# Kernel optimization log

Hardware: AMD Instinct MI355X
Metric: run time of the kernel (lower is better)

## Reference

```python
import jax, jax.numpy as jnp
import numpy as np

NEG = -1e9

def conv1x1(x, w, b):
    # x: [B,C,H,W], w: [O,C], b: [O]
    return jnp.einsum('bchw,oc->bohw', x, w) + b[None, :, None, None]


def setup_inputs() -> dict:
    key = jax.random.key(0)
    ks = jax.random.split(key, 12)
    B, C, H, W = 4, 512, 96, 96
    Cr = min(8, C // 8)  # = 8
    s = lambda fan: 1.0 / np.sqrt(fan)
    inp = {
        'x':   jax.random.normal(ks[0], (B, C, H, W), dtype=jnp.float32),
        'w_h': jax.random.normal(ks[1], (Cr, C), dtype=jnp.float32) * s(C),
        'b_h': jax.random.normal(ks[2], (Cr,), dtype=jnp.float32) * s(C),
        'w_w': jax.random.normal(ks[3], (Cr, C), dtype=jnp.float32) * s(C),
        'b_w': jax.random.normal(ks[4], (Cr,), dtype=jnp.float32) * s(C),
        'w_c': jax.random.normal(ks[5], (C, C), dtype=jnp.float32) * s(C),
        'b_c': jax.random.normal(ks[6], (C,), dtype=jnp.float32) * s(C),
        'w_o': jax.random.normal(ks[7], (C, C), dtype=jnp.float32) * s(C),
        'b_o': jax.random.normal(ks[8], (C,), dtype=jnp.float32) * s(C),
        # alpha/beta/gamma are nn.Parameter(zeros(1)); use small nonzero values
        # so all branches contribute to output/gradients.
        'alpha': jax.random.normal(ks[9], (1,), dtype=jnp.float32) * 0.1,
        'beta':  jax.random.normal(ks[10], (1,), dtype=jnp.float32) * 0.1,
        'gamma': jax.random.normal(ks[11], (1,), dtype=jnp.float32) * 0.1,
    }
    return inp


def reference(x, w_h, b_h, w_w, b_w, w_c, b_c, w_o, b_o, alpha, beta, gamma):
    B, C, H, W = x.shape
    f_hei = conv1x1(x, w_h, b_h)              # [B,Cr,H,W]
    Cr = f_hei.shape[1]
    # Faithful replication of torch permute/contiguous/view sequence
    # (the .view(B*W,-1,H) after permute reinterprets the (H,Cr) layout as (Cr,H)).
    f_h = f_hei.transpose(0, 3, 2, 1).reshape(B * W, Cr, H).transpose(0, 2, 1)  # [B*W,H,Cr]
    f_w = f_hei.transpose(0, 2, 1, 3).reshape(B * H, Cr, W).transpose(0, 2, 1)  # [B*H,W,Cr]
    f_wid = conv1x1(x, w_w, b_w)              # [B,Cr,H,W]
    ff_h = f_wid.transpose(0, 3, 1, 2).reshape(B * W, Cr, H)  # [B*W,Cr,H]
    ff_w = f_wid.transpose(0, 2, 1, 3).reshape(B * H, Cr, W)  # [B*H,Cr,W]
    # channel attention branch
    f_ch = conv1x1(x, w_c, b_c)               # [B,C,H,W]
    f_c = f_ch.reshape(B, C, H * W)           # [B,C,HW]
    ff_c = f_ch.transpose(0, 2, 3, 1).reshape(B, H * W, C)    # [B,HW,C]
    aff_c = jax.nn.softmax(jnp.matmul(f_c, ff_c), axis=2)     # [B,C,C]
    out_C = jnp.matmul(ff_c, aff_c).reshape(B, C, H, W)       # torch .view reinterpretation
    # axial (criss-cross) attention with masked concat-softmax
    E_h = jnp.matmul(f_h, ff_h)               # [B*W,H,H]
    E_h = E_h + (jnp.eye(H, dtype=x.dtype) * NEG)[None, :, :]
    E_h = E_h.reshape(B, W, H, H).transpose(0, 2, 1, 3)       # [B,H,W,H]
    E_w = jnp.matmul(f_w, ff_w).reshape(B, H, W, W)           # [B,H,W,W]
    concate = jax.nn.softmax(jnp.concatenate([E_h, E_w], axis=3), axis=3)  # [B,H,W,H+W]
    h_att = concate[:, :, :, :H].transpose(0, 2, 1, 3).reshape(B * W, H, H)
    w_att = concate[:, :, :, H:].reshape(B * H, W, W)
    f_cha = conv1x1(x, w_o, b_o)              # [B,C,H,W]
    P_H = f_cha.transpose(0, 3, 1, 2).reshape(B * W, C, H)
    P_W = f_cha.transpose(0, 2, 1, 3).reshape(B * H, C, W)
    out_H = jnp.matmul(P_H, h_att.transpose(0, 2, 1)).reshape(B, W, C, H).transpose(0, 2, 3, 1)
    out_W = jnp.matmul(P_W, w_att.transpose(0, 2, 1)).reshape(B, H, C, W).transpose(0, 2, 1, 3)
    return x + alpha * out_H + beta * out_W + gamma * out_C
```

## Files before the change

### kernel.cpp

```cpp
#include <hip/hip_runtime.h>

typedef __attribute__((ext_vector_type(8))) short short8;
typedef __attribute__((ext_vector_type(4))) float f32x4;
typedef __attribute__((ext_vector_type(4))) unsigned short us4;
typedef unsigned short u16;

#define kB 4
#define kC 512
#define kCr 8
#define kH 96
#define kW 96
#define kHW 9216
#define kCHW 4718592
#define NEGV -1e9f

__device__ __forceinline__ u16 f2b(float f) {
  union { float f; unsigned u; } v; v.f = f;
  unsigned r = v.u + 0x7fff + ((v.u >> 16) & 1);
  return (u16)(r >> 16);
}
__device__ __forceinline__ float b2f(u16 h) {
  union { unsigned u; float f; } v; v.u = ((unsigned)h) << 16;
  return v.f;
}
#define MFMA(a, b, c) __builtin_amdgcn_mfma_f32_16x16x32_bf16(a, b, c, 0, 0, 0)

__device__ __forceinline__ void gl16(const u16* g, u16* l) {
  __builtin_amdgcn_global_load_lds(
      (const __attribute__((address_space(1))) void*)g,
      (__attribute__((address_space(3))) void*)l, 16, 0, 0);
}

__global__ __launch_bounds__(256) void k_cvt_T(const float* __restrict__ in,
                                               u16* __restrict__ out,
                                               int R, int C) {
  const float* ib = in + (size_t)blockIdx.z * R * C;
  u16* ob = out + (size_t)blockIdx.z * R * C;
  int c0 = blockIdx.x * 64, r0 = blockIdx.y * 64;
  __shared__ u16 T[64][68];
  int tid = threadIdx.x;
#pragma unroll
  for (int p = 0; p < 4; p++) {
    int ch = tid + p * 256;
    int i = ch >> 4, seg = ch & 15;
    f32x4 v = *(const f32x4*)&ib[(size_t)(r0 + i) * C + c0 + seg * 4];
    T[i][seg*4+0] = f2b(v[0]); T[i][seg*4+1] = f2b(v[1]);
    T[i][seg*4+2] = f2b(v[2]); T[i][seg*4+3] = f2b(v[3]);
  }
  __syncthreads();
#pragma unroll
  for (int p = 0; p < 4; p++) {
    int ch = tid + p * 256;
    int j = ch >> 4, seg = ch & 15;
    us4 o;
#pragma unroll
    for (int e = 0; e < 4; e++) o[e] = T[seg*4+e][j];
    *(us4*)&ob[(size_t)(c0 + j) * R + r0 + seg * 4] = o;
  }
}

__global__ __launch_bounds__(256) void k_trT_bf(const u16* __restrict__ in,
                                                u16* __restrict__ out,
                                                int R, int C) {
  const u16* ib = in + (size_t)blockIdx.z * R * C;
  u16* ob = out + (size_t)blockIdx.z * R * C;
  int c0 = blockIdx.x * 64, r0 = blockIdx.y * 64;
  __shared__ u16 T[64][68];
  int tid = threadIdx.x;
#pragma unroll
  for (int p = 0; p < 4; p++) {
    int ch = tid + p * 256;
    int i = ch >> 4, seg = ch & 15;
    us4 v = *(const us4*)&ib[(size_t)(r0 + i) * C + c0 + seg * 4];
    T[i][seg*4+0] = v[0]; T[i][seg*4+1] = v[1];
    T[i][seg*4+2] = v[2]; T[i][seg*4+3] = v[3];
  }
  __syncthreads();
#pragma unroll
  for (int p = 0; p < 4; p++) {
    int ch = tid + p * 256;
    int j = ch >> 4, seg = ch & 15;
    us4 o;
#pragma unroll
    for (int e = 0; e < 4; e++) o[e] = T[seg*4+e][j];
    *(us4*)&ob[(size_t)(c0 + j) * R + r0 + seg * 4] = o;
  }
}

__global__ __launch_bounds__(256) void k_cvtw(const float* __restrict__ wc,
                                              const float* __restrict__ wo,
                                              u16* __restrict__ wco) {
  int i = blockIdx.x * 256 + threadIdx.x;
  const float* src = (i < 65536) ? &wc[(size_t)i * 4] : &wo[(size_t)(i - 65536) * 4];
  f32x4 v = *(const f32x4*)src;
  us4 o;
  o[0] = f2b(v[0]); o[1] = f2b(v[1]); o[2] = f2b(v[2]); o[3] = f2b(v[3]);
  ((us4*)wco)[i] = o;
}

__global__ __launch_bounds__(256) void k_conv16(
    const float* __restrict__ wh, const float* __restrict__ bh,
    const float* __restrict__ ww, const float* __restrict__ bw,
    const u16* __restrict__ XT, u16* __restrict__ Out) {
  __shared__ u16 As[16][520];
  __shared__ float bias_s[16];
  int tid = threadIdx.x;
#pragma unroll
  for (int p = 0; p < 4; p++) {
    int ch = tid + p * 256;
    int r = ch >> 6, seg = ch & 63;
    const float* src = (r < 8) ? &wh[r * 512 + seg * 8] : &ww[(r - 8) * 512 + seg * 8];
    f32x4 v0 = *(const f32x4*)src;
    f32x4 v1 = *(const f32x4*)(src + 4);
    short8 sv;
    sv[0]=f2b(v0[0]); sv[1]=f2b(v0[1]); sv[2]=f2b(v0[2]); sv[3]=f2b(v0[3]);
    sv[4]=f2b(v1[0]); sv[5]=f2b(v1[1]); sv[6]=f2b(v1[2]); sv[7]=f2b(v1[3]);
    *(short8*)&As[r][seg * 8] = sv;
  }
  if (tid < 16) bias_s[tid] = (tid < 8) ? bh[tid] : bw[tid - 8];
  __syncthreads();
  int b = blockIdx.y;
  int nb = blockIdx.x * 128 + (tid >> 6) * 32;
  int lane = tid & 63;
  int lr = lane & 15, lg = lane >> 4;
  const u16* Bb = XT + (size_t)b * kCHW;
  f32x4 acc[2] = {};
#pragma unroll 4
  for (int k0 = 0; k0 < 512; k0 += 32) {
    short8 a = *(const short8*)&As[lr][k0 + lg * 8];
    short8 b0 = *(const short8*)&Bb[(size_t)(nb + lr) * 512 + k0 + lg * 8];
    short8 b1 = *(const short8*)&Bb[(size_t)(nb + 16 + lr) * 512 + k0 + lg * 8];
    acc[0] = MFMA(a, b0, acc[0]);
    acc[1] = MFMA(a, b1, acc[1]);
  }
#pragma unroll
  for (int q = 0; q < 2; q++)
#pragma unroll
    for (int r = 0; r < 4; r++) {
      int m = lg * 4 + r;
      Out[((size_t)b * 16 + m) * kHW + nb + q * 16 + lr] = f2b(acc[q][r] + bias_s[m]);
    }
}

#define GEMM_PROLOG()                                                      \
  int tid = threadIdx.x;                                                   \
  int lane = tid & 63, wv = tid >> 6;                                      \
  int wr = (wv >> 1) * 64, wc = (wv & 1) * 64;                             \
  int lr = lane & 15, lg = lane >> 4;                                      \
  f32x4 acc[4][4] = {};

#define STAGE(bufv, kk)                                                    \
  {                                                                        \
    _Pragma("unroll")                                                      \
    for (int p = 0; p < 4; p++) {                                          \
      int ch = tid + p * 256;                                              \
      int row = ch >> 3, cc = ch & 7;                                      \
      int sc = (cc ^ (row & 7)) * 8;                                       \
      gl16(&Asrc[(size_t)(bm + row) * LDA + (kk) + sc], &As[bufv][row][cc * 8]); \
      gl16(&Bsrc[(size_t)(bn + row) * LDB + (kk) + sc], &Bs[bufv][row][cc * 8]); \
    }                                                                      \
  }

#define COMPUTE(bufv)                                                      \
  {                                                                        \
    _Pragma("unroll")                                                      \
    for (int ks = 0; ks < 2; ks++) {                                       \
      int ca = ((ks * 4 + lg) ^ (lr & 7)) * 8;                             \
      short8 av[4], bv[4];                                                 \
      _Pragma("unroll")                                                    \
      for (int m = 0; m < 4; m++)                                          \
        av[m] = *(const short8*)&As[bufv][wr + m * 16 + lr][ca];           \
      _Pragma("unroll")                                                    \
      for (int n = 0; n < 4; n++)                                          \
        bv[n] = *(const short8*)&Bs[bufv][wc + n * 16 + lr][ca];           \
      __builtin_amdgcn_s_setprio(1);                                       \
      _Pragma("unroll")                                                    \
      for (int m = 0; m < 4; m++)                                          \
        _Pragma("unroll")                                                  \
        for (int n = 0; n < 4; n++)                                        \
          acc[m][n] = MFMA(av[m], bv[n], acc[m][n]);                       \
      __builtin_amdgcn_s_setprio(0);                                       \
    }                                                                      \
  }

#define VMBAR(N)                                                           \
  asm volatile("s_waitcnt vmcnt(" #N ")" ::: "memory");                    \
  __builtin_amdgcn_s_barrier();

#define LGBAR                                                              \
  asm volatile("s_waitcnt lgkmcnt(0)" ::: "memory");                       \
  __builtin_amdgcn_s_barrier();

#define PIPELOOP(NT, KBASE)                                                \
  STAGE(0, (KBASE));                                                       \
  STAGE(1, (KBASE) + 64);                                                  \
  {                                                                        \
    int cur = 0;                                                           \
    _Pragma("unroll 1")                                                    \
    for (int t = 0; t < (NT) - 2; t++) {                                   \
      VMBAR(8);                                                            \
      COMPUTE(cur);                                                        \
      LGBAR;                                                               \
      STAGE(cur, (KBASE) + (t + 2) * 64);                                  \
      cur ^= 1;                                                            \
    }                                                                      \
    VMBAR(8);                                                              \
    COMPUTE(cur);                                                          \
    cur ^= 1;                                                              \
    VMBAR(0);                                                              \
    COMPUTE(cur);                                                          \
  }

__global__ __launch_bounds__(256) void k_gemm_conv2(
    const u16* __restrict__ wco, const u16* __restrict__ BT,
    const float* __restrict__ b_c, const float* __restrict__ b_o,
    u16* __restrict__ f_ch, u16* __restrict__ f_cha) {
  __shared__ u16 As[2][128][64];
  __shared__ u16 Bs[2][128][64];
  int b = blockIdx.z;
  int bm = blockIdx.y * 128;
  int bn = blockIdx.x * 128;
  const u16* Asrc = wco;
  const u16* Bsrc = BT + (size_t)b * kCHW;
  const int LDA = 512, LDB = 512;
  GEMM_PROLOG();
  PIPELOOP(8, 0);
  const float* biasp = (bm < 512) ? (b_c + bm) : (b_o + bm - 512);
  u16* Ob = (bm < 512) ? (f_ch + (size_t)b * kCHW + (size_t)bm * kHW)
                       : (f_cha + (size_t)b * kCHW + (size_t)(bm - 512) * kHW);
#pragma unroll
  for (int m = 0; m < 4; m++)
#pragma unroll
    for (int r = 0; r < 4; r++) {
      int ol = wr + m * 16 + lg * 4 + r;
      float bv_ = biasp[ol];
#pragma unroll
      for (int n = 0; n < 4; n++)
        Ob[(size_t)ol * kHW + bn + wc + n * 16 + lr] = f2b(acc[m][n][r] + bv_);
    }
}

__global__ __launch_bounds__(256) void k_gram_sk(const u16* __restrict__ F,
                                                 u16* __restrict__ part) {
  __shared__ u16 As[2][128][64];
  __shared__ u16 Bs[2][128][64];
  int z = blockIdx.z;
  int b = z & 3, s = z >> 2;
  int bm = blockIdx.y * 128, bn = blockIdx.x * 128;
  const u16* Asrc = F + (size_t)b * kCHW;
  const u16* Bsrc = Asrc;
  const int LDA = kHW, LDB = kHW;
  int kbeg = s * 1152;
  GEMM_PROLOG();
  PIPELOOP(18, kbeg);
  u16* Pb = part + ((size_t)(s * 4 + b)) * 262144;
#pragma unroll
  for (int m = 0; m < 4; m++)
#pragma unroll
    for (int r = 0; r < 4; r++) {
      int i = bm + wr + m * 16 + lg * 4 + r;
#pragma unroll
      for (int n = 0; n < 4; n++)
        Pb[(size_t)i * 512 + bn + wc + n * 16 + lr] = f2b(acc[m][n][r]);
    }
}

__global__ __launch_bounds__(256) void k_outc(
    const u16* __restrict__ AT, const u16* __restrict__ Bt,
    const float* __restrict__ gamma, u16* __restrict__ Out) {
  __shared__ u16 As[2][128][64];
  __shared__ u16 Bs[2][128][64];
  int b = blockIdx.z;
  int bm = blockIdx.y * 128;
  int bn = blockIdx.x * 128;
  const u16* Asrc = AT + (size_t)b * kCHW;
  const u16* Bsrc = Bt + (size_t)b * 262144;
  const int LDA = 512, LDB = 512;
  GEMM_PROLOG();
  PIPELOOP(8, 0);
  float g = *gamma;
  u16* Ob = Out + (size_t)b * kCHW;
#pragma unroll
  for (int m = 0; m < 4; m++)
#pragma unroll
    for (int r = 0; r < 4; r++) {
      int mm = bm + wr + m * 16 + lg * 4 + r;
#pragma unroll
      for (int n = 0; n < 4; n++)
        Ob[(size_t)mm * 512 + bn + wc + n * 16 + lr] = f2b(g * acc[m][n][r]);
    }
}

__global__ __launch_bounds__(256) void k_softmax512r(const u16* __restrict__ part,
                                                     float* __restrict__ gramN) {
  int b = blockIdx.x >> 9, i = blockIdx.x & 511;
  int tid = threadIdx.x;
  float v0 = 0.f, v1 = 0.f;
#pragma unroll
  for (int s = 0; s < 8; s++) {
    const u16* P = part + ((size_t)(s * 4 + b) * 512 + i) * 512;
    v0 += b2f(P[tid]);
    v1 += b2f(P[tid + 256]);
  }
  int wid = tid >> 6, lane = tid & 63;
  float m = fmaxf(v0, v1);
#pragma unroll
  for (int o = 32; o >= 1; o >>= 1) m = fmaxf(m, __shfl_xor(m, o));
  __shared__ float redm[4], reds[4];
  if (lane == 0) redm[wid] = m;
  __syncthreads();
  m = fmaxf(fmaxf(redm[0], redm[1]), fmaxf(redm[2], redm[3]));
  float e0 = expf(v0 - m), e1 = expf(v1 - m);
  float s = e0 + e1;
#pragma unroll
  for (int o = 32; o >= 1; o >>= 1) s += __shfl_xor(s, o);
  if (lane == 0) reds[wid] = s;
  __syncthreads();
  s = reds[0] + reds[1] + reds[2] + reds[3];
  float inv = 1.0f / s;
  float* R = gramN + ((size_t)b * 512 + i) * 512;
  R[tid] = e0 * inv;
  R[tid + 256] = e1 * inv;
}

__global__ __launch_bounds__(256) void k_eh(
    const u16* __restrict__ fhw, u16* __restrict__ Ccat) {
  int b = blockIdx.x / kW, w = blockIdx.x % kW;
  __shared__ float fh[kH][kCr];
  __shared__ float fw[kCr][kH];
  int tid = threadIdx.x;
  for (int l = tid; l < kH * kCr; l += 256) {
    int i = l >> 3, c = l & 7;
    fh[i][c] = b2f(fhw[((size_t)b * 16 + (i & 7)) * kHW + (c * 12 + (i >> 3)) * kW + w]);
    int c2 = l / kH, j = l % kH;
    fw[c2][j] = b2f(fhw[((size_t)b * 16 + 8 + c2) * kHW + j * kW + w]);
  }
  __syncthreads();
  for (int t = tid; t < kH * kH; t += 256) {
    int i = t / kH, j = t % kH;
    float e = 0.f;
#pragma unroll
    for (int c = 0; c < kCr; c++) e += fh[i][c] * fw[c][j];
    if (i == j) e += NEGV;
    Ccat[(((size_t)b * kH + i) * kW + w) * 192 + j] = f2b(e);
  }
}

__global__ __launch_bounds__(256) void k_ew(
    const u16* __restrict__ fhw, u16* __restrict__ Ccat) {
  int b = blockIdx.x / kH, h = blockIdx.x % kH;
  __shared__ float fh2[kCr][kW];
  __shared__ float fw2[kCr][kW];
  int tid = threadIdx.x;
  for (int l = tid; l < kCr * kW; l += 256) {
    int c = l / kW, w = l % kW;
    fh2[c][w] = b2f(fhw[((size_t)b * 16 + c) * kHW + h * kW + w]);
    fw2[c][w] = b2f(fhw[((size_t)b * 16 + 8 + c) * kHW + h * kW + w]);
  }
  __syncthreads();
  for (int t = tid; t < kW * kW; t += 256) {
    int w = t / kW, j = t % kW;
    float e = 0.f;
#pragma unroll
    for (int c = 0; c < kCr; c++) e += fh2[c][w] * fw2[c][j];
    Ccat[(((size_t)b * kH + h) * kW + w) * 192 + 96 + j] = f2b(e);
  }
}

__global__ __launch_bounds__(256) void k_softmax192(u16* __restrict__ Ccat) {
  int r = blockIdx.x * 4 + (threadIdx.x >> 6);
  int lane = threadIdx.x & 63;
  u16* R = Ccat + (size_t)r * 192;
  float a = b2f(R[lane]), b = b2f(R[lane + 64]), c = b2f(R[lane + 128]);
  float m = fmaxf(a, fmaxf(b, c));
#pragma unroll
  for (int o = 32; o >= 1; o >>= 1) m = fmaxf(m, __shfl_xor(m, o));
  float ea = expf(a - m), eb = expf(b - m), ec = expf(c - m);
  float s = ea + eb + ec;
#pragma unroll
  for (int o = 32; o >= 1; o >>= 1) s += __shfl_xor(s, o);
  float inv = 1.0f / s;
  R[lane] = f2b(ea * inv);
  R[lane + 64] = f2b(eb * inv);
  R[lane + 128] = f2b(ec * inv);
}

__global__ __launch_bounds__(256) void k_tr_plane(const u16* __restrict__ in,
                                                  u16* __restrict__ out) {
  size_t pl = blockIdx.x;
  const u16* ib = in + pl * 9216;
  u16* ob = out + pl * 9216;
  __shared__ u16 T[96][100];
  int tid = threadIdx.x;
  for (int ch = tid; ch < 96 * 24; ch += 256) {
    int i = ch / 24, seg = ch % 24;
    *(us4*)&T[i][seg*4] = *(const us4*)&ib[i*96 + seg*4];
  }
  __syncthreads();
  for (int ch = tid; ch < 96 * 24; ch += 256) {
    int j = ch / 24, seg = ch % 24;
    us4 o;
#pragma unroll
    for (int e = 0; e < 4; e++) o[e] = T[seg*4+e][j];
    *(us4*)&ob[j*96 + seg*4] = o;
  }
}

__global__ __launch_bounds__(512) void k_final_h(
    const u16* __restrict__ AT,
    const u16* __restrict__ att,
    const float* __restrict__ alpha,
    u16* __restrict__ OutHT) {
  int b = blockIdx.x / 96, w = blockIdx.x % 96;
  __shared__ u16 Bs[96][104];
  int tid = threadIdx.x;
  for (int ch = tid; ch < 1152; ch += 512) {
    int h = ch / 12, seg = ch % 12;
    *(short8*)&Bs[h][seg*8] =
        *(const short8*)&att[(((size_t)b*96 + h)*96 + w)*192 + seg*8];
  }
  __syncthreads();
  int lane = tid & 63, wv = tid >> 6;
  int lr = lane & 15, lg = lane >> 4;
  int c0 = wv * 64;
  const u16* Ab = AT + ((size_t)b*512 + c0)*kHW + w*96;
  f32x4 acc[4][6] = {};
#pragma unroll
  for (int ks = 0; ks < 3; ks++) {
    short8 av[4];
#pragma unroll
    for (int m = 0; m < 4; m++)
      av[m] = *(const short8*)&Ab[(size_t)(m*16 + lr)*kHW + ks*32 + lg*8];
#pragma unroll
    for (int n = 0; n < 6; n++) {
      short8 bv = *(const short8*)&Bs[n*16 + lr][ks*32 + lg*8];
#pragma unroll
      for (int m = 0; m < 4; m++) acc[m][n] = MFMA(av[m], bv, acc[m][n]);
    }
  }
  float al = *alpha;
  u16* Ob = OutHT + ((size_t)b*512 + c0)*kHW + w*96;
#pragma unroll
  for (int m = 0; m < 4; m++)
#pragma unroll
    for (int r = 0; r < 4; r++) {
      size_t crow = (size_t)(m*16 + lg*4 + r) * kHW;
#pragma unroll
      for (int n = 0; n < 6; n++)
        Ob[crow + n*16 + lr] = f2b(al * acc[m][n][r]);
    }
}

__global__ __launch_bounds__(512) void k_final_w(
    const u16* __restrict__ A,
    const u16* __restrict__ att,
    const float* __restrict__ beta,
    u16* __restrict__ OutW) {
  int b = blockIdx.x / 96, h = blockIdx.x % 96;
  __shared__ u16 Bs[96][104];
  int tid = threadIdx.x;
  for (int ch = tid; ch < 1152; ch += 512) {
    int wr_ = ch / 12, seg = ch % 12;
    *(short8*)&Bs[wr_][seg*8] =
        *(const short8*)&att[(((size_t)b*96 + h)*96 + wr_)*192 + 96 + seg*8];
  }
  __syncthreads();
  int lane = tid & 63, wv = tid >> 6;
  int lr = lane & 15, lg = lane >> 4;
  int c0 = wv * 64;
  const u16* Ab = A + ((size_t)b*512 + c0)*kHW + h*96;
  f32x4 acc[4][6] = {};
#pragma unroll
  for (int ks = 0; ks < 3; ks++) {
    short8 av[4];
#pragma unroll
    for (int m = 0; m < 4; m++)
      av[m] = *(const short8*)&Ab[(size_t)(m*16 + lr)*kHW + ks*32 + lg*8];
#pragma unroll
    for (int n = 0; n < 6; n++) {
      short8 bv = *(const short8*)&Bs[n*16 + lr][ks*32 + lg*8];
#pragma unroll
      for (int m = 0; m < 4; m++) acc[m][n] = MFMA(av[m], bv, acc[m][n]);
    }
  }
  float be = *beta;
  u16* Ob = OutW + ((size_t)b*512 + c0)*kHW + h*96;
#pragma unroll
  for (int m = 0; m < 4; m++)
#pragma unroll
    for (int r = 0; r < 4; r++) {
      size_t crow = (size_t)(m*16 + lg*4 + r) * kHW;
#pragma unroll
      for (int n = 0; n < 6; n++)
        Ob[crow + n*16 + lr] = f2b(be * acc[m][n][r]);
    }
}

__global__ __launch_bounds__(256) void k_merge(
    const float* __restrict__ x, const u16* __restrict__ OutC,
    const u16* __restrict__ OutW, const u16* __restrict__ HT,
    float* __restrict__ out) {
  size_t pl = blockIdx.x;
  const u16* hb = HT + pl * 9216;
  __shared__ u16 T[96][100];
  int tid = threadIdx.x;
  for (int ch = tid; ch < 96 * 24; ch += 256) {
    int i = ch / 24, seg = ch % 24;
    *(us4*)&T[i][seg*4] = *(const us4*)&hb[i*96 + seg*4];
  }
  __syncthreads();
  const float* xb = x + pl * 9216;
  const u16* cb = OutC + pl * 9216;
  const u16* wb = OutW + pl * 9216;
  float* ob = out + pl * 9216;
  for (int ch = tid; ch < 2304; ch += 256) {
    int i4 = ch * 4;
    int h = i4 / 96, w = i4 % 96;
    f32x4 xv = *(const f32x4*)&xb[i4];
    us4 cv = *(const us4*)&cb[i4];
    us4 wv = *(const us4*)&wb[i4];
    f32x4 o;
#pragma unroll
    for (int e = 0; e < 4; e++)
      o[e] = xv[e] + b2f(cv[e]) + b2f(wv[e]) + b2f(T[w + e][h]);
    *(f32x4*)&ob[i4] = o;
  }
}

extern "C" void kernel_launch(void* const* d_in, const int* in_sizes, int n_in,
                              void* d_out, int out_size, void* d_ws, size_t ws_size,
                              hipStream_t stream) {
  const float* x     = (const float*)d_in[0];
  const float* w_h   = (const float*)d_in[1];
  const float* b_h   = (const float*)d_in[2];
  const float* w_w   = (const float*)d_in[3];
  const float* b_w   = (const float*)d_in[4];
  const float* w_c   = (const float*)d_in[5];
  const float* b_c   = (const float*)d_in[6];
  const float* w_o   = (const float*)d_in[7];
  const float* b_o   = (const float*)d_in[8];
  const float* alpha = (const float*)d_in[9];
  const float* beta  = (const float*)d_in[10];
  const float* gamma = (const float*)d_in[11];
  float* out = (float*)d_out;

  const size_t R = 37748736;
  char* p = (char*)d_ws;
  u16*   xbfT   = (u16*)(p);
  u16*   part   = (u16*)(p);
  u16*   f_chaT = (u16*)(p);
  u16*   outW   = (u16*)(p);
  u16*   f_ch   = (u16*)(p + R);
  u16*   outC   = (u16*)(p + R);
  u16*   f_chT  = (u16*)(p + 2 * R);
  u16*   outHT  = (u16*)(p + 2 * R);
  u16*   f_cha  = (u16*)(p + 3 * R);
  u16*   fhw    = (u16*)(p + 4 * R);
  char*  F      = p + 4 * R + 2359296;
  float* gramN  = (float*)F;
  u16*   affT   = (u16*)(F + 4194304);
  u16*   ccat   = (u16*)F;
  u16*   wco    = (u16*)(F + 14155776);

  k_cvt_T<<<dim3(144, 8, 4), 256, 0, stream>>>(x, xbfT, 512, 9216);
  k_cvtw<<<512, 256, 0, stream>>>(w_c, w_o, wco);
  k_conv16<<<dim3(72, 4), 256, 0, stream>>>(w_h, b_h, w_w, b_w, xbfT, fhw);
  k_gemm_conv2<<<dim3(72, 8, 4), 256, 0, stream>>>(wco, xbfT, b_c, b_o, f_ch, f_cha);
  k_trT_bf<<<dim3(144, 8, 4), 256, 0, stream>>>(f_ch, f_chT, 512, 9216);
  k_gram_sk<<<dim3(4, 4, 32), 256, 0, stream>>>(f_ch, part);
  k_softmax512r<<<2048, 256, 0, stream>>>(part, gramN);
  k_cvt_T<<<dim3(8, 8, 4), 256, 0, stream>>>(gramN, affT, 512, 512);
  k_outc<<<dim3(4, 72, 4), 256, 0, stream>>>(f_chT, affT, gamma, outC);
  k_eh<<<384, 256, 0, stream>>>(fhw, ccat);
  k_ew<<<384, 256, 0, stream>>>(fhw, ccat);
  k_softmax192<<<9216, 256, 0, stream>>>(ccat);
  k_tr_plane<<<2048, 256, 0, stream>>>(f_cha, f_chaT);
  k_final_h<<<384, 512, 0, stream>>>(f_chaT, ccat, alpha, outHT);
  k_final_w<<<384, 512, 0, stream>>>(f_cha, ccat, beta, outW);
  k_merge<<<2048, 256, 0, stream>>>(x, outC, outW, outHT, out);
}
```

Before: 304.9 us.

## Fuse f_ch transpose into conv GEMM, exploit Gram symmetry, widen N tiles

The channel conv GEMM now loops over four 128-wide N segments per block and writes both f_ch and its transpose directly from registers. This removes the separate k_trT_bf transpose pass over a 4.7M-element tensor per batch. The Gram split-K kernel computes only the upper-triangular 128x128 tiles (10 of 16) and mirrors the off-diagonal ones with transposed stores. k_outc processes two N segments per block so the pipeline prologue is amortized. The costs are strided transposed stores that may coalesce poorly and fewer blocks per launch.

```diff
diff --git a/kernel.cpp b/kernel.cpp
--- a/kernel.cpp
+++ b/kernel.cpp
@@ -46,34 +46,6 @@
     f32x4 v = *(const f32x4*)&ib[(size_t)(r0 + i) * C + c0 + seg * 4];
     T[i][seg*4+0] = f2b(v[0]); T[i][seg*4+1] = f2b(v[1]);
     T[i][seg*4+2] = f2b(v[2]); T[i][seg*4+3] = f2b(v[3]);
-  }
-  __syncthreads();
-#pragma unroll
-  for (int p = 0; p < 4; p++) {
-    int ch = tid + p * 256;
-    int j = ch >> 4, seg = ch & 15;
-    us4 o;
-#pragma unroll
-    for (int e = 0; e < 4; e++) o[e] = T[seg*4+e][j];
-    *(us4*)&ob[(size_t)(c0 + j) * R + r0 + seg * 4] = o;
-  }
-}
-
-__global__ __launch_bounds__(256) void k_trT_bf(const u16* __restrict__ in,
-                                                u16* __restrict__ out,
-                                                int R, int C) {
-  const u16* ib = in + (size_t)blockIdx.z * R * C;
-  u16* ob = out + (size_t)blockIdx.z * R * C;
-  int c0 = blockIdx.x * 64, r0 = blockIdx.y * 64;
-  __shared__ u16 T[64][68];
-  int tid = threadIdx.x;
-#pragma unroll
-  for (int p = 0; p < 4; p++) {
-    int ch = tid + p * 256;
-    int i = ch >> 4, seg = ch & 15;
-    us4 v = *(const us4*)&ib[(size_t)(r0 + i) * C + c0 + seg * 4];
-    T[i][seg*4+0] = v[0]; T[i][seg*4+1] = v[1];
-    T[i][seg*4+2] = v[2]; T[i][seg*4+3] = v[3];
   }
   __syncthreads();
 #pragma unroll
@@ -214,30 +186,69 @@
 __global__ __launch_bounds__(256) void k_gemm_conv2(
     const u16* __restrict__ wco, const u16* __restrict__ BT,
     const float* __restrict__ b_c, const float* __restrict__ b_o,
-    u16* __restrict__ f_ch, u16* __restrict__ f_cha) {
+    u16* __restrict__ f_ch, u16* __restrict__ f_cha, u16* __restrict__ f_chT) {
   __shared__ u16 As[2][128][64];
   __shared__ u16 Bs[2][128][64];
   int b = blockIdx.z;
   int bm = blockIdx.y * 128;
-  int bn = blockIdx.x * 128;
+  int bn0 = blockIdx.x * 512;
   const u16* Asrc = wco;
   const u16* Bsrc = BT + (size_t)b * kCHW;
-  const int LDA = 512, LDB = 512;
   GEMM_PROLOG();
-  PIPELOOP(8, 0);
   const float* biasp = (bm < 512) ? (b_c + bm) : (b_o + bm - 512);
+  float bias_r[16];
+#pragma unroll
+  for (int m = 0; m < 4; m++)
+#pragma unroll
+    for (int r = 0; r < 4; r++)
+      bias_r[m * 4 + r] = biasp[wr + m * 16 + lg * 4 + r];
   u16* Ob = (bm < 512) ? (f_ch + (size_t)b * kCHW + (size_t)bm * kHW)
                        : (f_cha + (size_t)b * kCHW + (size_t)(bm - 512) * kHW);
-#pragma unroll
-  for (int m = 0; m < 4; m++)
-#pragma unroll
-    for (int r = 0; r < 4; r++) {
-      int ol = wr + m * 16 + lg * 4 + r;
-      float bv_ = biasp[ol];
-#pragma unroll
-      for (int n = 0; n < 4; n++)
-        Ob[(size_t)ol * kHW + bn + wc + n * 16 + lr] = f2b(acc[m][n][r] + bv_);
-    }
+  u16* Tb = f_chT + (size_t)b * kCHW;
+
+#define C2_STAGE(bufv, t)                                                  \
+  {                                                                        \
+    int seg_ = (t) >> 3, kk_ = ((t) & 7) * 64;                             \
+    int bn_ = bn0 + seg_ * 128;                                            \
+    _Pragma("unroll")                                                      \
+    for (int p = 0; p < 4; p++) {                                          \
+      int ch = tid + p * 256;                                              \
+      int row = ch >> 3, cc = ch & 7;                                      \
+      int sc = (cc ^ (row & 7)) * 8;                                       \
+      gl16(&Asrc[(size_t)(bm + row) * 512 + kk_ + sc], &As[bufv][row][cc * 8]); \
+      gl16(&Bsrc[(size_t)(bn_ + row) * 512 + kk_ + sc], &Bs[bufv][row][cc * 8]); \
+    }                                                                      \
+  }
+
+  C2_STAGE(0, 0);
+  C2_STAGE(1, 1);
+  int cur = 0;
+#pragma unroll 1
+  for (int t = 0; t < 32; t++) {
+    if (t < 31) { VMBAR(8); } else { VMBAR(0); }
+    COMPUTE(cur);
+    if (t < 30) { LGBAR; C2_STAGE(cur, t + 2); }
+    cur ^= 1;
+    if ((t & 7) == 7) {
+      int bn = bn0 + (t >> 3) * 128;
+#pragma unroll
+      for (int m = 0; m < 4; m++)
+#pragma unroll
+        for (int n = 0; n < 4; n++) {
+          us4 tv;
+#pragma unroll
+          for (int r = 0; r < 4; r++) {
+            float v = acc[m][n][r] + bias_r[m * 4 + r];
+            tv[r] = f2b(v);
+            Ob[(size_t)(wr + m * 16 + lg * 4 + r) * kHW + bn + wc + n * 16 + lr] = tv[r];
+            acc[m][n][r] = 0.f;
+          }
+          if (bm < 512)
+            *(us4*)&Tb[(size_t)(bn + wc + n * 16 + lr) * 512 + bm + wr + m * 16 + lg * 4] = tv;
+        }
+    }
+  }
+#undef C2_STAGE
 }
 
 __global__ __launch_bounds__(256) void k_gram_sk(const u16* __restrict__ F,
@@ -246,7 +257,9 @@
   __shared__ u16 Bs[2][128][64];
   int z = blockIdx.z;
   int b = z & 3, s = z >> 2;
-  int bm = blockIdx.y * 128, bn = blockIdx.x * 128;
+  int L = blockIdx.x;
+  int bm = (int)((0x3221110000ull >> (4 * L)) & 15) * 128;
+  int bn = (int)((0x3323213210ull >> (4 * L)) & 15) * 128;
   const u16* Asrc = F + (size_t)b * kCHW;
   const u16* Bsrc = Asrc;
   const int LDA = kHW, LDB = kHW;
@@ -257,11 +270,15 @@
 #pragma unroll
   for (int m = 0; m < 4; m++)
 #pragma unroll
-    for (int r = 0; r < 4; r++) {
-      int i = bm + wr + m * 16 + lg * 4 + r;
-#pragma unroll
-      for (int n = 0; n < 4; n++)
-        Pb[(size_t)i * 512 + bn + wc + n * 16 + lr] = f2b(acc[m][n][r]);
+    for (int n = 0; n < 4; n++) {
+      us4 tv;
+#pragma unroll
+      for (int r = 0; r < 4; r++) {
+        tv[r] = f2b(acc[m][n][r]);
+        Pb[(size_t)(bm + wr + m * 16 + lg * 4 + r) * 512 + bn + wc + n * 16 + lr] = tv[r];
+      }
+      if (bm != bn)
+        *(us4*)&Pb[(size_t)(bn + wc + n * 16 + lr) * 512 + bm + wr + m * 16 + lg * 4] = tv;
     }
 }
 
@@ -272,23 +289,52 @@
   __shared__ u16 Bs[2][128][64];
   int b = blockIdx.z;
   int bm = blockIdx.y * 128;
-  int bn = blockIdx.x * 128;
+  int bn0 = blockIdx.x * 256;
   const u16* Asrc = AT + (size_t)b * kCHW;
   const u16* Bsrc = Bt + (size_t)b * 262144;
-  const int LDA = 512, LDB = 512;
   GEMM_PROLOG();
-  PIPELOOP(8, 0);
   float g = *gamma;
   u16* Ob = Out + (size_t)b * kCHW;
-#pragma unroll
-  for (int m = 0; m < 4; m++)
-#pragma unroll
-    for (int r = 0; r < 4; r++) {
-      int mm = bm + wr + m * 16 + lg * 4 + r;
-#pragma unroll
-      for (int n = 0; n < 4; n++)
-        Ob[(size_t)mm * 512 + bn + wc + n * 16 + lr] = f2b(g * acc[m][n][r]);
-    }
+
+#define OC_STAGE(bufv, t)                                                  \
+  {                                                                        \
+    int seg_ = (t) >> 3, kk_ = ((t) & 7) * 64;                             \
+    int bn_ = bn0 + seg_ * 128;                                            \
+    _Pragma("unroll")                                                      \
+    for (int p = 0; p < 4; p++) {                                          \
+      int ch = tid + p * 256;                                              \
+      int row = ch >> 3, cc = ch & 7;                                      \
+      int sc = (cc ^ (row & 7)) * 8;                                       \
+      gl16(&Asrc[(size_t)(bm + row) * 512 + kk_ + sc], &As[bufv][row][cc * 8]); \
+      gl16(&Bsrc[(size_t)(bn_ + row) * 512 + kk_ + sc], &Bs[bufv][row][cc * 8]); \
+    }                                                                      \
+  }
+
+  OC_STAGE(0, 0);
+  OC_STAGE(1, 1);
+  int cur = 0;
+#pragma unroll 1
+  for (int t = 0; t < 16; t++) {
+    if (t < 15) { VMBAR(8); } else { VMBAR(0); }
+    COMPUTE(cur);
+    if (t < 14) { LGBAR; OC_STAGE(cur, t + 2); }
+    cur ^= 1;
+    if ((t & 7) == 7) {
+      int bn = bn0 + (t >> 3) * 128;
+#pragma unroll
+      for (int m = 0; m < 4; m++)
+#pragma unroll
+        for (int r = 0; r < 4; r++) {
+          int mm = bm + wr + m * 16 + lg * 4 + r;
+#pragma unroll
+          for (int n = 0; n < 4; n++) {
+            Ob[(size_t)mm * 512 + bn + wc + n * 16 + lr] = f2b(g * acc[m][n][r]);
+            acc[m][n][r] = 0.f;
+          }
+        }
+    }
+  }
+#undef OC_STAGE
 }
 
 __global__ __launch_bounds__(256) void k_softmax512r(const u16* __restrict__ part,
@@ -565,12 +611,11 @@
   k_cvt_T<<<dim3(144, 8, 4), 256, 0, stream>>>(x, xbfT, 512, 9216);
   k_cvtw<<<512, 256, 0, stream>>>(w_c, w_o, wco);
   k_conv16<<<dim3(72, 4), 256, 0, stream>>>(w_h, b_h, w_w, b_w, xbfT, fhw);
-  k_gemm_conv2<<<dim3(72, 8, 4), 256, 0, stream>>>(wco, xbfT, b_c, b_o, f_ch, f_cha);
-  k_trT_bf<<<dim3(144, 8, 4), 256, 0, stream>>>(f_ch, f_chT, 512, 9216);
-  k_gram_sk<<<dim3(4, 4, 32), 256, 0, stream>>>(f_ch, part);
+  k_gemm_conv2<<<dim3(18, 8, 4), 256, 0, stream>>>(wco, xbfT, b_c, b_o, f_ch, f_cha, f_chT);
+  k_gram_sk<<<dim3(10, 1, 32), 256, 0, stream>>>(f_ch, part);
   k_softmax512r<<<2048, 256, 0, stream>>>(part, gramN);
   k_cvt_T<<<dim3(8, 8, 4), 256, 0, stream>>>(gramN, affT, 512, 512);
-  k_outc<<<dim3(4, 72, 4), 256, 0, stream>>>(f_chT, affT, gamma, outC);
+  k_outc<<<dim3(2, 72, 4), 256, 0, stream>>>(f_chT, affT, gamma, outC);
   k_eh<<<384, 256, 0, stream>>>(fhw, ccat);
   k_ew<<<384, 256, 0, stream>>>(fhw, ccat);
   k_softmax192<<<9216, 256, 0, stream>>>(ccat);
```

Result: slower. 337.0 us (+10.5%).

## Fuse f_ch transpose into conv GEMM epilogue and exploit Gram symmetry

Applied to the files above, without the earlier changes.

The conv GEMM epilogue now also writes a transposed copy of f_ch through shared memory, which removes the separate k_trT_bf transpose kernel and its extra read/write pass. The Gram split-K kernel computes only the upper-triangular 128x128 tiles (10 of 16) and mirrors each tile into its symmetric position, cutting its MFMA work. The costs are a larger epilogue with extra syncs and LDS traffic in the conv kernel, and uncoalesced mirrored stores in the Gram kernel. The tvals array is computed but never used.

```diff
diff --git a/kernel.cpp b/kernel.cpp
--- a/kernel.cpp
+++ b/kernel.cpp
@@ -46,34 +46,6 @@
     f32x4 v = *(const f32x4*)&ib[(size_t)(r0 + i) * C + c0 + seg * 4];
     T[i][seg*4+0] = f2b(v[0]); T[i][seg*4+1] = f2b(v[1]);
     T[i][seg*4+2] = f2b(v[2]); T[i][seg*4+3] = f2b(v[3]);
-  }
-  __syncthreads();
-#pragma unroll
-  for (int p = 0; p < 4; p++) {
-    int ch = tid + p * 256;
-    int j = ch >> 4, seg = ch & 15;
-    us4 o;
-#pragma unroll
-    for (int e = 0; e < 4; e++) o[e] = T[seg*4+e][j];
-    *(us4*)&ob[(size_t)(c0 + j) * R + r0 + seg * 4] = o;
-  }
-}
-
-__global__ __launch_bounds__(256) void k_trT_bf(const u16* __restrict__ in,
-                                                u16* __restrict__ out,
-                                                int R, int C) {
-  const u16* ib = in + (size_t)blockIdx.z * R * C;
-  u16* ob = out + (size_t)blockIdx.z * R * C;
-  int c0 = blockIdx.x * 64, r0 = blockIdx.y * 64;
-  __shared__ u16 T[64][68];
-  int tid = threadIdx.x;
-#pragma unroll
-  for (int p = 0; p < 4; p++) {
-    int ch = tid + p * 256;
-    int i = ch >> 4, seg = ch & 15;
-    us4 v = *(const us4*)&ib[(size_t)(r0 + i) * C + c0 + seg * 4];
-    T[i][seg*4+0] = v[0]; T[i][seg*4+1] = v[1];
-    T[i][seg*4+2] = v[2]; T[i][seg*4+3] = v[3];
   }
   __syncthreads();
 #pragma unroll
@@ -214,9 +186,10 @@
 __global__ __launch_bounds__(256) void k_gemm_conv2(
     const u16* __restrict__ wco, const u16* __restrict__ BT,
     const float* __restrict__ b_c, const float* __restrict__ b_o,
-    u16* __restrict__ f_ch, u16* __restrict__ f_cha) {
-  __shared__ u16 As[2][128][64];
-  __shared__ u16 Bs[2][128][64];
+    u16* __restrict__ f_ch, u16* __restrict__ f_cha, u16* __restrict__ f_chT) {
+  __shared__ u16 smem[32768];
+  u16 (*As)[128][64] = (u16 (*)[128][64])smem;
+  u16 (*Bs)[128][64] = (u16 (*)[128][64])(smem + 16384);
   int b = blockIdx.z;
   int bm = blockIdx.y * 128;
   int bn = blockIdx.x * 128;
@@ -228,6 +201,7 @@
   const float* biasp = (bm < 512) ? (b_c + bm) : (b_o + bm - 512);
   u16* Ob = (bm < 512) ? (f_ch + (size_t)b * kCHW + (size_t)bm * kHW)
                        : (f_cha + (size_t)b * kCHW + (size_t)(bm - 512) * kHW);
+  u16 tvals[4][4];
 #pragma unroll
   for (int m = 0; m < 4; m++)
 #pragma unroll
@@ -235,9 +209,37 @@
       int ol = wr + m * 16 + lg * 4 + r;
       float bv_ = biasp[ol];
 #pragma unroll
-      for (int n = 0; n < 4; n++)
-        Ob[(size_t)ol * kHW + bn + wc + n * 16 + lr] = f2b(acc[m][n][r] + bv_);
-    }
+      for (int n = 0; n < 4; n++) {
+        u16 hv = f2b(acc[m][n][r] + bv_);
+        Ob[(size_t)ol * kHW + bn + wc + n * 16 + lr] = hv;
+        tvals[m][n] = (r == 0) ? hv : tvals[m][n];
+      }
+    }
+  if (bm < 512) {
+    __syncthreads();
+    u16 (*T)[136] = (u16 (*)[136])smem;
+#pragma unroll
+    for (int m = 0; m < 4; m++)
+#pragma unroll
+      for (int n = 0; n < 4; n++) {
+        int ol = wr + m * 16 + lg * 4;
+        float bv0 = biasp[ol], bv1 = biasp[ol+1], bv2 = biasp[ol+2], bv3 = biasp[ol+3];
+        int nl = wc + n * 16 + lr;
+        T[nl][ol + 0] = f2b(acc[m][n][0] + bv0);
+        T[nl][ol + 1] = f2b(acc[m][n][1] + bv1);
+        T[nl][ol + 2] = f2b(acc[m][n][2] + bv2);
+        T[nl][ol + 3] = f2b(acc[m][n][3] + bv3);
+      }
+    __syncthreads();
+    u16* Tb = f_chT + (size_t)b * kCHW;
+#pragma unroll
+    for (int p = 0; p < 16; p++) {
+      int ch = tid + p * 256;
+      int row = ch >> 5, seg = ch & 31;
+      us4 v = *(const us4*)&T[row][seg * 4];
+      *(us4*)&Tb[(size_t)(bn + row) * 512 + bm + seg * 4] = v;
+    }
+  }
 }
 
 __global__ __launch_bounds__(256) void k_gram_sk(const u16* __restrict__ F,
@@ -246,7 +248,9 @@
   __shared__ u16 Bs[2][128][64];
   int z = blockIdx.z;
   int b = z & 3, s = z >> 2;
-  int bm = blockIdx.y * 128, bn = blockIdx.x * 128;
+  int L = blockIdx.x;
+  int bm = (int)((0x3221110000ull >> (4 * L)) & 15) * 128;
+  int bn = (int)((0x3323213210ull >> (4 * L)) & 15) * 128;
   const u16* Asrc = F + (size_t)b * kCHW;
   const u16* Bsrc = Asrc;
   const int LDA = kHW, LDB = kHW;
@@ -257,11 +261,15 @@
 #pragma unroll
   for (int m = 0; m < 4; m++)
 #pragma unroll
-    for (int r = 0; r < 4; r++) {
-      int i = bm + wr + m * 16 + lg * 4 + r;
-#pragma unroll
-      for (int n = 0; n < 4; n++)
-        Pb[(size_t)i * 512 + bn + wc + n * 16 + lr] = f2b(acc[m][n][r]);
+    for (int n = 0; n < 4; n++) {
+      us4 tv;
+#pragma unroll
+      for (int r = 0; r < 4; r++) {
+        tv[r] = f2b(acc[m][n][r]);
+        Pb[(size_t)(bm + wr + m * 16 + lg * 4 + r) * 512 + bn + wc + n * 16 + lr] = tv[r];
+      }
+      if (bm != bn)
+        *(us4*)&Pb[(size_t)(bn + wc + n * 16 + lr) * 512 + bm + wr + m * 16 + lg * 4] = tv;
     }
 }
 
@@ -565,9 +573,8 @@
   k_cvt_T<<<dim3(144, 8, 4), 256, 0, stream>>>(x, xbfT, 512, 9216);
   k_cvtw<<<512, 256, 0, stream>>>(w_c, w_o, wco);
   k_conv16<<<dim3(72, 4), 256, 0, stream>>>(w_h, b_h, w_w, b_w, xbfT, fhw);
-  k_gemm_conv2<<<dim3(72, 8, 4), 256, 0, stream>>>(wco, xbfT, b_c, b_o, f_ch, f_cha);
-  k_trT_bf<<<dim3(144, 8, 4), 256, 0, stream>>>(f_ch, f_chT, 512, 9216);
-  k_gram_sk<<<dim3(4, 4, 32), 256, 0, stream>>>(f_ch, part);
+  k_gemm_conv2<<<dim3(72, 8, 4), 256, 0, stream>>>(wco, xbfT, b_c, b_o, f_ch, f_cha, f_chT);
+  k_gram_sk<<<dim3(10, 1, 32), 256, 0, stream>>>(f_ch, part);
   k_softmax512r<<<2048, 256, 0, stream>>>(part, gramN);
   k_cvt_T<<<dim3(8, 8, 4), 256, 0, stream>>>(gramN, affT, 512, 512);
   k_outc<<<dim3(4, 72, 4), 256, 0, stream>>>(f_chT, affT, gamma, outC);
```

Measured after the change: 294.0 us. 1.04x faster.
